# Performance work log

Hardware: AMD Instinct MI355X
Metric: run time of the kernel (lower is better)

## Reference

```python
import jax, jax.numpy as jnp
import numpy as np

N = 100000
E = 1600000
DIN = 128
HID = 128
EPS = 1e-5


def setup_inputs() -> dict:
    key = jax.random.key(0)
    ks = jax.random.split(key, 16)
    s = lambda i, shape, sc=0.05: jax.random.normal(ks[i], shape, dtype=jnp.float32) * sc
    inp = {
        "x": jax.random.normal(ks[0], (N, DIN), dtype=jnp.float32),
        "edge_index": jax.random.randint(ks[1], (2, E), 0, N, dtype=jnp.int64),
        # layer 1
        "W1": s(2, (DIN, HID)), "b1": jnp.zeros((HID,), jnp.float32),
        "g1": jnp.ones((HID,), jnp.float32), "be1": jnp.zeros((HID,), jnp.float32),
        "m1": s(3, (HID,)), "v1": jax.random.uniform(ks[4], (HID,), jnp.float32) + 0.5,
        # layer 2
        "W2": s(5, (HID, HID)), "b2": jnp.zeros((HID,), jnp.float32),
        "g2": jnp.ones((HID,), jnp.float32), "be2": jnp.zeros((HID,), jnp.float32),
        "m2": s(6, (HID,)), "v2": jax.random.uniform(ks[7], (HID,), jnp.float32) + 0.5,
        # classifier
        "Wc1": s(8, (HID, HID // 2)), "bc1": jnp.zeros((HID // 2,), jnp.float32),
        "Wc2": s(9, (HID // 2, 2)), "bc2": jnp.zeros((2,), jnp.float32),
    }
    return inp


def _gnn_layer(x, W, b, src, dst):
    # linear then scatter-mean of source features onto destinations
    h = x @ W + b                                    # [N, HID]
    msg_sum = jax.ops.segment_sum(h[src], dst, num_segments=N)   # [N, HID]
    cnt = jax.ops.segment_sum(jnp.ones((src.shape[0],), h.dtype), dst, num_segments=N)
    return msg_sum / cnt[:, None]                    # self-loops guarantee cnt >= 1


def _bn(x, g, be, m, v):
    return (x - m) * jax.lax.rsqrt(v + EPS) * g + be


def reference(x, edge_index, W1, b1, g1, be1, m1, v1, W2, b2, g2, be2, m2, v2, Wc1, bc1, Wc2, bc2):
    # add self loops (PyG add_self_loops appends [i, i])
    loop = jnp.arange(N, dtype=edge_index.dtype)
    src = jnp.concatenate([edge_index[0], loop])
    dst = jnp.concatenate([edge_index[1], loop])

    h = _gnn_layer(x, W1, b1, src, dst)
    h = jax.nn.relu(_bn(h, g1, be1, m1, v1))
    h = _gnn_layer(h, W2, b2, src, dst)
    h = jax.nn.relu(_bn(h, g2, be2, m2, v2))

    h = jax.nn.relu(h @ Wc1 + bc1)
    return h @ Wc2 + bc2                              # logits [N, 2]
```

## Files before the change

kernel.cpp:

```cpp
#include <hip/hip_runtime.h>
#include <hip/hip_bf16.h>

#define EPS 1e-5f

__global__ __launch_bounds__(256) void k_zero(int* p, int n) {
    int i = blockIdx.x * 256 + threadIdx.x;
    if (i < n) p[i] = 0;
}

__global__ __launch_bounds__(256) void k_histrank(const int* __restrict__ dst,
                                                  int* __restrict__ counts,
                                                  int* __restrict__ rank, int nE) {
    int i = blockIdx.x * 256 + threadIdx.x;
    if (i < nE) rank[i] = atomicAdd(&counts[dst[i]], 1);
}

__global__ __launch_bounds__(256) void k_scan1(const int* __restrict__ counts,
                                               int* __restrict__ bsums, int n) {
    __shared__ int sdata[256];
    int base = blockIdx.x * 2048;
    int t = threadIdx.x;
    int s = 0;
#pragma unroll
    for (int i = 0; i < 8; ++i) {
        int idx = base + t * 8 + i;
        if (idx < n) s += counts[idx];
    }
    sdata[t] = s;
    __syncthreads();
    for (int off = 128; off > 0; off >>= 1) {
        if (t < off) sdata[t] += sdata[t + off];
        __syncthreads();
    }
    if (t == 0) bsums[blockIdx.x] = sdata[0];
}

__global__ __launch_bounds__(64) void k_scan2(int* __restrict__ bsums, int nb) {
    if (threadIdx.x == 0 && blockIdx.x == 0) {
        int acc = 0;
        for (int i = 0; i < nb; ++i) { int v = bsums[i]; bsums[i] = acc; acc += v; }
    }
}

__global__ __launch_bounds__(256) void k_scan3(const int* __restrict__ counts,
                                               const int* __restrict__ bsums,
                                               int* __restrict__ rowstart,
                                               int n, int nE) {
    __shared__ int sth[256];
    int base = blockIdx.x * 2048;
    int t = threadIdx.x;
    int loc[8];
    int s = 0;
#pragma unroll
    for (int i = 0; i < 8; ++i) {
        int idx = base + t * 8 + i;
        loc[i] = s;
        s += (idx < n) ? counts[idx] : 0;
    }
    sth[t] = s;
    __syncthreads();
    for (int off = 1; off < 256; off <<= 1) {
        int tmp = (t >= off) ? sth[t - off] : 0;
        __syncthreads();
        sth[t] += tmp;
        __syncthreads();
    }
    int excl = sth[t] - s + bsums[blockIdx.x];
#pragma unroll
    for (int i = 0; i < 8; ++i) {
        int idx = base + t * 8 + i;
        if (idx < n) rowstart[idx] = excl + loc[i];
    }
    if (blockIdx.x == 0 && t == 0) rowstart[n] = nE;
}

__global__ __launch_bounds__(256) void k_fill3(const int* __restrict__ srci,
                                               const int* __restrict__ dsti,
                                               const int* __restrict__ rank,
                                               const int* __restrict__ rowstart,
                                               int* __restrict__ col, int nE) {
    int e = blockIdx.x * 256 + threadIdx.x;
    if (e < nE) {
        col[rowstart[dsti[e]] + rank[e]] = srci[e];
    }
}

__global__ __launch_bounds__(256) void k_linear(const float* __restrict__ X,
                                                const float* __restrict__ W,
                                                const float* __restrict__ bias,
                                                float* __restrict__ out,
                                                int nRows) {
    __shared__ float xs[64][132];
    int row0 = blockIdx.x * 64;
    int tid = threadIdx.x;
    for (int i = tid; i < 64 * 32; i += 256) {
        int r = i >> 5, c4 = (i & 31) << 2;
        float4 v = make_float4(0.f, 0.f, 0.f, 0.f);
        int row = row0 + r;
        if (row < nRows) v = *(const float4*)(X + (size_t)row * 128 + c4);
        *(float4*)&xs[r][c4] = v;
    }
    __syncthreads();

    int cg = tid & 15, rg = tid >> 4;
    int c0 = cg * 8, r0 = rg * 4;
    float acc[4][8];
    float4 b0 = *(const float4*)(bias + c0);
    float4 b1 = *(const float4*)(bias + c0 + 4);
#pragma unroll
    for (int r = 0; r < 4; ++r) {
        acc[r][0] = b0.x; acc[r][1] = b0.y; acc[r][2] = b0.z; acc[r][3] = b0.w;
        acc[r][4] = b1.x; acc[r][5] = b1.y; acc[r][6] = b1.z; acc[r][7] = b1.w;
    }

    for (int k0 = 0; k0 < 128; k0 += 4) {
        float4 xv[4];
#pragma unroll
        for (int r = 0; r < 4; ++r) xv[r] = *(const float4*)&xs[r0 + r][k0];
#pragma unroll
        for (int kk = 0; kk < 4; ++kk) {
            int k = k0 + kk;
            float4 w0 = *(const float4*)(W + k * 128 + c0);
            float4 w1 = *(const float4*)(W + k * 128 + c0 + 4);
            float wv[8] = {w0.x, w0.y, w0.z, w0.w, w1.x, w1.y, w1.z, w1.w};
#pragma unroll
            for (int r = 0; r < 4; ++r) {
                float xk = (&xv[r].x)[kk];
#pragma unroll
                for (int j = 0; j < 8; ++j) acc[r][j] = fmaf(xk, wv[j], acc[r][j]);
            }
        }
    }

#pragma unroll
    for (int r = 0; r < 4; ++r) {
        int row = row0 + r0 + r;
        if (row >= nRows) continue;
        *(float4*)(out + (size_t)row * 128 + c0) =
            make_float4(acc[r][0], acc[r][1], acc[r][2], acc[r][3]);
        *(float4*)(out + (size_t)row * 128 + c0 + 4) =
            make_float4(acc[r][4], acc[r][5], acc[r][6], acc[r][7]);
    }
}

template <bool FUSE_BN>
__global__ __launch_bounds__(256) void k_gather(const float* __restrict__ src,
                                                const int* __restrict__ rowstart,
                                                const int* __restrict__ col,
                                                const float* __restrict__ g,
                                                const float* __restrict__ be,
                                                const float* __restrict__ m,
                                                const float* __restrict__ v,
                                                float* __restrict__ out, int nRows) {
    int r = blockIdx.x * 4 + (threadIdx.x >> 6);
    if (r >= nRows) return;
    int lane = threadIdx.x & 63;
    int d0 = lane * 2;
    int s = rowstart[r], e = rowstart[r + 1];

    float2 acc = *(const float2*)(src + (size_t)r * 128 + d0);
    int j = s;
    for (; j + 8 <= e; j += 8) {
        int ci[8];
#pragma unroll
        for (int u = 0; u < 8; ++u) ci[u] = col[j + u];
        float2 t[8];
#pragma unroll
        for (int u = 0; u < 8; ++u)
            t[u] = *(const float2*)(src + (size_t)ci[u] * 128 + d0);
#pragma unroll
        for (int u = 0; u < 8; ++u) { acc.x += t[u].x; acc.y += t[u].y; }
    }
    for (; j < e; ++j) {
        int ci = col[j];
        float2 a = *(const float2*)(src + (size_t)ci * 128 + d0);
        acc.x += a.x;
        acc.y += a.y;
    }
    float rc = 1.0f / (float)(e - s + 1);
    float2 o;
    if (FUSE_BN) {
        float2 gv = *(const float2*)(g + d0);
        float2 bev = *(const float2*)(be + d0);
        float2 mv = *(const float2*)(m + d0);
        float2 vv = *(const float2*)(v + d0);
        o.x = fmaxf((acc.x * rc - mv.x) * rsqrtf(vv.x + EPS) * gv.x + bev.x, 0.f);
        o.y = fmaxf((acc.y * rc - mv.y) * rsqrtf(vv.y + EPS) * gv.y + bev.y, 0.f);
    } else {
        o.x = acc.x * rc;
        o.y = acc.y * rc;
    }
    *(float2*)(out + (size_t)r * 128 + d0) = o;
}

__global__ __launch_bounds__(256) void k_final(const float* __restrict__ xin,
                                               const float* __restrict__ Wc1,
                                               const float* __restrict__ bc1,
                                               const float* __restrict__ Wc2,
                                               const float* __restrict__ bc2,
                                               float* __restrict__ out, int nRows) {
    __shared__ float xs[32][132];
    __shared__ float w1s[128][64];
    __shared__ float hs[32][68];
    int row0 = blockIdx.x * 32;
    int tid = threadIdx.x;

    for (int i = tid; i < 2048; i += 256) {
        int kk = i >> 4, c4 = (i & 15) << 2;
        *(float4*)&w1s[kk][c4] = *(const float4*)(Wc1 + kk * 64 + c4);
    }
    for (int i = tid; i < 1024; i += 256) {
        int r = i >> 5, c4 = (i & 31) << 2;
        int row = row0 + r;
        float4 o = make_float4(0.f, 0.f, 0.f, 0.f);
        if (row < nRows) o = *(const float4*)(xin + (size_t)row * 128 + c4);
        *(float4*)&xs[r][c4] = o;
    }
    __syncthreads();

    int cg = tid & 15, rg = tid >> 4;
    int c0 = cg * 4, r0 = rg * 2;
    float acc[2][4];
    float4 bc = *(const float4*)(bc1 + c0);
    acc[0][0] = bc.x; acc[0][1] = bc.y; acc[0][2] = bc.z; acc[0][3] = bc.w;
    acc[1][0] = bc.x; acc[1][1] = bc.y; acc[1][2] = bc.z; acc[1][3] = bc.w;
    for (int k = 0; k < 128; ++k) {
        float4 w4 = *(const float4*)&w1s[k][c0];
        float x0 = xs[r0][k], x1 = xs[r0 + 1][k];
        acc[0][0] = fmaf(x0, w4.x, acc[0][0]);
        acc[0][1] = fmaf(x0, w4.y, acc[0][1]);
        acc[0][2] = fmaf(x0, w4.z, acc[0][2]);
        acc[0][3] = fmaf(x0, w4.w, acc[0][3]);
        acc[1][0] = fmaf(x1, w4.x, acc[1][0]);
        acc[1][1] = fmaf(x1, w4.y, acc[1][1]);
        acc[1][2] = fmaf(x1, w4.z, acc[1][2]);
        acc[1][3] = fmaf(x1, w4.w, acc[1][3]);
    }
    *(float4*)&hs[r0][c0] = make_float4(fmaxf(acc[0][0], 0.f), fmaxf(acc[0][1], 0.f),
                                        fmaxf(acc[0][2], 0.f), fmaxf(acc[0][3], 0.f));
    *(float4*)&hs[r0 + 1][c0] = make_float4(fmaxf(acc[1][0], 0.f), fmaxf(acc[1][1], 0.f),
                                            fmaxf(acc[1][2], 0.f), fmaxf(acc[1][3], 0.f));
    __syncthreads();

    if (tid < 64) {
        int r = tid >> 1, oc = tid & 1;
        float s = bc2[oc];
        for (int c = 0; c < 64; ++c) s = fmaf(hs[r][c], Wc2[c * 2 + oc], s);
        int row = row0 + r;
        if (row < nRows) out[(size_t)row * 2 + oc] = s;
    }
}

extern "C" void kernel_launch(void* const* d_in, const int* in_sizes, int n_in,
                              void* d_out, int out_size, void* d_ws, size_t ws_size,
                              hipStream_t stream) {
    const float* x   = (const float*)d_in[0];
    const int*   ei  = (const int*)d_in[1];
    const float* W1  = (const float*)d_in[2];
    const float* b1  = (const float*)d_in[3];
    const float* g1  = (const float*)d_in[4];
    const float* be1 = (const float*)d_in[5];
    const float* m1  = (const float*)d_in[6];
    const float* v1  = (const float*)d_in[7];
    const float* W2  = (const float*)d_in[8];
    const float* b2  = (const float*)d_in[9];
    const float* g2  = (const float*)d_in[10];
    const float* be2 = (const float*)d_in[11];
    const float* m2  = (const float*)d_in[12];
    const float* v2  = (const float*)d_in[13];
    const float* Wc1 = (const float*)d_in[14];
    const float* bc1 = (const float*)d_in[15];
    const float* Wc2 = (const float*)d_in[16];
    const float* bc2 = (const float*)d_in[17];

    const int N_ = in_sizes[0] / 128;
    const int E_ = in_sizes[1] / 2;
    const int* srci = ei;
    const int* dsti = ei + E_;

    float* A = (float*)d_ws;
    float* B = A + (size_t)N_ * 128;
    int* rank = (int*)B;
    int* counts   = (int*)(B + (size_t)N_ * 128);
    int* rowstart = counts + N_;
    int* bsums    = rowstart + N_ + 1;
    int* col      = bsums + 256;

    const int nb = (N_ + 2047) / 2048;

    k_zero    <<<(N_ + 255) / 256, 256, 0, stream>>>(counts, N_);
    k_histrank<<<(E_ + 255) / 256, 256, 0, stream>>>(dsti, counts, rank, E_);
    k_scan1   <<<nb, 256, 0, stream>>>(counts, bsums, N_);
    k_scan2   <<<1, 64, 0, stream>>>(bsums, nb);
    k_scan3   <<<nb, 256, 0, stream>>>(counts, bsums, rowstart, N_, E_);
    k_fill3   <<<(E_ + 255) / 256, 256, 0, stream>>>(srci, dsti, rank, rowstart,
                                                     col, E_);

    k_linear<<<(N_ + 63) / 64, 256, 0, stream>>>(x, W1, b1, A, N_);
    k_gather<true><<<(N_ + 3) / 4, 256, 0, stream>>>(A, rowstart, col,
                                                     g1, be1, m1, v1, B, N_);

    k_linear<<<(N_ + 63) / 64, 256, 0, stream>>>(B, W2, b2, A, N_);
    k_gather<true><<<(N_ + 3) / 4, 256, 0, stream>>>(A, rowstart, col,
                                                     g2, be2, m2, v2, B, N_);

    k_final<<<(N_ + 31) / 32, 256, 0, stream>>>(B, Wc1, bc1, Wc2, bc2,
                                                (float*)d_out, N_);
}
```

Measured before the change: 630.4 us.

## Fuse gather+BN with next linear layer and with classifier head

Merges each neighbor-gather/batchnorm/relu kernel with the following dense layer (W2 linear, or the two-layer classifier head). Aggregated rows go into shared memory and are multiplied directly, so the intermediate N×128 tensor is no longer written to and re-read from global memory. Weights are now read from global/L1 per k-step instead of being staged in LDS. Also replaces the zeroing kernel with hipMemsetAsync and makes the rank store nontemporal.

```diff
diff --git a/kernel.cpp b/kernel.cpp
--- a/kernel.cpp
+++ b/kernel.cpp
@@ -2,17 +2,15 @@
 #include <hip/hip_bf16.h>
 
 #define EPS 1e-5f
-
-__global__ __launch_bounds__(256) void k_zero(int* p, int n) {
-    int i = blockIdx.x * 256 + threadIdx.x;
-    if (i < n) p[i] = 0;
-}
 
 __global__ __launch_bounds__(256) void k_histrank(const int* __restrict__ dst,
                                                   int* __restrict__ counts,
                                                   int* __restrict__ rank, int nE) {
     int i = blockIdx.x * 256 + threadIdx.x;
-    if (i < nE) rank[i] = atomicAdd(&counts[dst[i]], 1);
+    if (i < nE) {
+        int p = atomicAdd(&counts[dst[i]], 1);
+        __builtin_nontemporal_store(p, &rank[i]);
+    }
 }
 
 __global__ __launch_bounds__(256) void k_scan1(const int* __restrict__ counts,
@@ -143,103 +141,176 @@
     }
 }
 
-template <bool FUSE_BN>
-__global__ __launch_bounds__(256) void k_gather(const float* __restrict__ src,
-                                                const int* __restrict__ rowstart,
-                                                const int* __restrict__ col,
-                                                const float* __restrict__ g,
-                                                const float* __restrict__ be,
-                                                const float* __restrict__ m,
-                                                const float* __restrict__ v,
-                                                float* __restrict__ out, int nRows) {
-    int r = blockIdx.x * 4 + (threadIdx.x >> 6);
-    if (r >= nRows) return;
-    int lane = threadIdx.x & 63;
+__global__ __launch_bounds__(512) void k_glin(const float* __restrict__ src,
+                                              const int* __restrict__ rowstart,
+                                              const int* __restrict__ col,
+                                              const float* __restrict__ g,
+                                              const float* __restrict__ be,
+                                              const float* __restrict__ m,
+                                              const float* __restrict__ v,
+                                              const float* __restrict__ W,
+                                              const float* __restrict__ bias,
+                                              float* __restrict__ out, int nRows) {
+    __shared__ float xs[32][132];
+    int row0 = blockIdx.x * 32;
+    int tid = threadIdx.x;
+    int wid = tid >> 6, lane = tid & 63;
     int d0 = lane * 2;
-    int s = rowstart[r], e = rowstart[r + 1];
-
-    float2 acc = *(const float2*)(src + (size_t)r * 128 + d0);
-    int j = s;
-    for (; j + 8 <= e; j += 8) {
-        int ci[8];
-#pragma unroll
-        for (int u = 0; u < 8; ++u) ci[u] = col[j + u];
-        float2 t[8];
-#pragma unroll
-        for (int u = 0; u < 8; ++u)
-            t[u] = *(const float2*)(src + (size_t)ci[u] * 128 + d0);
-#pragma unroll
-        for (int u = 0; u < 8; ++u) { acc.x += t[u].x; acc.y += t[u].y; }
-    }
-    for (; j < e; ++j) {
-        int ci = col[j];
-        float2 a = *(const float2*)(src + (size_t)ci * 128 + d0);
-        acc.x += a.x;
-        acc.y += a.y;
-    }
-    float rc = 1.0f / (float)(e - s + 1);
-    float2 o;
-    if (FUSE_BN) {
-        float2 gv = *(const float2*)(g + d0);
-        float2 bev = *(const float2*)(be + d0);
-        float2 mv = *(const float2*)(m + d0);
-        float2 vv = *(const float2*)(v + d0);
-        o.x = fmaxf((acc.x * rc - mv.x) * rsqrtf(vv.x + EPS) * gv.x + bev.x, 0.f);
-        o.y = fmaxf((acc.y * rc - mv.y) * rsqrtf(vv.y + EPS) * gv.y + bev.y, 0.f);
-    } else {
-        o.x = acc.x * rc;
-        o.y = acc.y * rc;
-    }
-    *(float2*)(out + (size_t)r * 128 + d0) = o;
-}
-
-__global__ __launch_bounds__(256) void k_final(const float* __restrict__ xin,
+
+    float2 gv  = *(const float2*)(g + d0);
+    float2 bev = *(const float2*)(be + d0);
+    float2 mv  = *(const float2*)(m + d0);
+    float2 vv  = *(const float2*)(v + d0);
+    float sx = rsqrtf(vv.x + EPS) * gv.x;
+    float sy = rsqrtf(vv.y + EPS) * gv.y;
+
+#pragma unroll
+    for (int rr = 0; rr < 4; ++rr) {
+        int lr = wid * 4 + rr;
+        int r = row0 + lr;
+        float2 o = make_float2(0.f, 0.f);
+        if (r < nRows) {
+            int s = rowstart[r], e = rowstart[r + 1];
+            float2 acc = *(const float2*)(src + (size_t)r * 128 + d0);
+            int j = s;
+            for (; j + 8 <= e; j += 8) {
+                int ci[8];
+#pragma unroll
+                for (int u = 0; u < 8; ++u) ci[u] = col[j + u];
+                float2 t[8];
+#pragma unroll
+                for (int u = 0; u < 8; ++u)
+                    t[u] = *(const float2*)(src + (size_t)ci[u] * 128 + d0);
+#pragma unroll
+                for (int u = 0; u < 8; ++u) { acc.x += t[u].x; acc.y += t[u].y; }
+            }
+            for (; j < e; ++j) {
+                int ci = col[j];
+                float2 a = *(const float2*)(src + (size_t)ci * 128 + d0);
+                acc.x += a.x; acc.y += a.y;
+            }
+            float rc = 1.0f / (float)(e - s + 1);
+            o.x = fmaxf((acc.x * rc - mv.x) * sx + bev.x, 0.f);
+            o.y = fmaxf((acc.y * rc - mv.y) * sy + bev.y, 0.f);
+        }
+        *(float2*)&xs[lr][d0] = o;
+    }
+    __syncthreads();
+
+    int cg = tid & 15, rg = tid >> 4;
+    int c0 = cg * 8;
+    float acc[8];
+    float4 b0 = *(const float4*)(bias + c0);
+    float4 b1 = *(const float4*)(bias + c0 + 4);
+    acc[0] = b0.x; acc[1] = b0.y; acc[2] = b0.z; acc[3] = b0.w;
+    acc[4] = b1.x; acc[5] = b1.y; acc[6] = b1.z; acc[7] = b1.w;
+
+    for (int k0 = 0; k0 < 128; k0 += 4) {
+        float4 xv = *(const float4*)&xs[rg][k0];
+#pragma unroll
+        for (int kk = 0; kk < 4; ++kk) {
+            int k = k0 + kk;
+            float4 w0 = *(const float4*)(W + k * 128 + c0);
+            float4 w1 = *(const float4*)(W + k * 128 + c0 + 4);
+            float xk = (&xv.x)[kk];
+            acc[0] = fmaf(xk, w0.x, acc[0]);
+            acc[1] = fmaf(xk, w0.y, acc[1]);
+            acc[2] = fmaf(xk, w0.z, acc[2]);
+            acc[3] = fmaf(xk, w0.w, acc[3]);
+            acc[4] = fmaf(xk, w1.x, acc[4]);
+            acc[5] = fmaf(xk, w1.y, acc[5]);
+            acc[6] = fmaf(xk, w1.z, acc[6]);
+            acc[7] = fmaf(xk, w1.w, acc[7]);
+        }
+    }
+
+    int orow = row0 + rg;
+    if (orow < nRows) {
+        *(float4*)(out + (size_t)orow * 128 + c0) =
+            make_float4(acc[0], acc[1], acc[2], acc[3]);
+        *(float4*)(out + (size_t)orow * 128 + c0 + 4) =
+            make_float4(acc[4], acc[5], acc[6], acc[7]);
+    }
+}
+
+__global__ __launch_bounds__(512) void k_ghead(const float* __restrict__ src,
+                                               const int* __restrict__ rowstart,
+                                               const int* __restrict__ col,
+                                               const float* __restrict__ g,
+                                               const float* __restrict__ be,
+                                               const float* __restrict__ m,
+                                               const float* __restrict__ v,
                                                const float* __restrict__ Wc1,
                                                const float* __restrict__ bc1,
                                                const float* __restrict__ Wc2,
                                                const float* __restrict__ bc2,
                                                float* __restrict__ out, int nRows) {
     __shared__ float xs[32][132];
-    __shared__ float w1s[128][64];
     __shared__ float hs[32][68];
     int row0 = blockIdx.x * 32;
     int tid = threadIdx.x;
-
-    for (int i = tid; i < 2048; i += 256) {
-        int kk = i >> 4, c4 = (i & 15) << 2;
-        *(float4*)&w1s[kk][c4] = *(const float4*)(Wc1 + kk * 64 + c4);
-    }
-    for (int i = tid; i < 1024; i += 256) {
-        int r = i >> 5, c4 = (i & 31) << 2;
-        int row = row0 + r;
-        float4 o = make_float4(0.f, 0.f, 0.f, 0.f);
-        if (row < nRows) o = *(const float4*)(xin + (size_t)row * 128 + c4);
-        *(float4*)&xs[r][c4] = o;
+    int wid = tid >> 6, lane = tid & 63;
+    int d0 = lane * 2;
+
+    float2 gv  = *(const float2*)(g + d0);
+    float2 bev = *(const float2*)(be + d0);
+    float2 mv  = *(const float2*)(m + d0);
+    float2 vv  = *(const float2*)(v + d0);
+    float sx = rsqrtf(vv.x + EPS) * gv.x;
+    float sy = rsqrtf(vv.y + EPS) * gv.y;
+
+#pragma unroll
+    for (int rr = 0; rr < 4; ++rr) {
+        int lr = wid * 4 + rr;
+        int r = row0 + lr;
+        float2 o = make_float2(0.f, 0.f);
+        if (r < nRows) {
+            int s = rowstart[r], e = rowstart[r + 1];
+            float2 acc = *(const float2*)(src + (size_t)r * 128 + d0);
+            int j = s;
+            for (; j + 8 <= e; j += 8) {
+                int ci[8];
+#pragma unroll
+                for (int u = 0; u < 8; ++u) ci[u] = col[j + u];
+                float2 t[8];
+#pragma unroll
+                for (int u = 0; u < 8; ++u)
+                    t[u] = *(const float2*)(src + (size_t)ci[u] * 128 + d0);
+#pragma unroll
+                for (int u = 0; u < 8; ++u) { acc.x += t[u].x; acc.y += t[u].y; }
+            }
+            for (; j < e; ++j) {
+                int ci = col[j];
+                float2 a = *(const float2*)(src + (size_t)ci * 128 + d0);
+                acc.x += a.x; acc.y += a.y;
+            }
+            float rc = 1.0f / (float)(e - s + 1);
+            o.x = fmaxf((acc.x * rc - mv.x) * sx + bev.x, 0.f);
+            o.y = fmaxf((acc.y * rc - mv.y) * sy + bev.y, 0.f);
+        }
+        *(float2*)&xs[lr][d0] = o;
     }
     __syncthreads();
 
     int cg = tid & 15, rg = tid >> 4;
-    int c0 = cg * 4, r0 = rg * 2;
-    float acc[2][4];
+    int c0 = cg * 4;
+    float acc[4];
     float4 bc = *(const float4*)(bc1 + c0);
-    acc[0][0] = bc.x; acc[0][1] = bc.y; acc[0][2] = bc.z; acc[0][3] = bc.w;
-    acc[1][0] = bc.x; acc[1][1] = bc.y; acc[1][2] = bc.z; acc[1][3] = bc.w;
-    for (int k = 0; k < 128; ++k) {
-        float4 w4 = *(const float4*)&w1s[k][c0];
-        float x0 = xs[r0][k], x1 = xs[r0 + 1][k];
-        acc[0][0] = fmaf(x0, w4.x, acc[0][0]);
-        acc[0][1] = fmaf(x0, w4.y, acc[0][1]);
-        acc[0][2] = fmaf(x0, w4.z, acc[0][2]);
-        acc[0][3] = fmaf(x0, w4.w, acc[0][3]);
-        acc[1][0] = fmaf(x1, w4.x, acc[1][0]);
-        acc[1][1] = fmaf(x1, w4.y, acc[1][1]);
-        acc[1][2] = fmaf(x1, w4.z, acc[1][2]);
-        acc[1][3] = fmaf(x1, w4.w, acc[1][3]);
-    }
-    *(float4*)&hs[r0][c0] = make_float4(fmaxf(acc[0][0], 0.f), fmaxf(acc[0][1], 0.f),
-                                        fmaxf(acc[0][2], 0.f), fmaxf(acc[0][3], 0.f));
-    *(float4*)&hs[r0 + 1][c0] = make_float4(fmaxf(acc[1][0], 0.f), fmaxf(acc[1][1], 0.f),
-                                            fmaxf(acc[1][2], 0.f), fmaxf(acc[1][3], 0.f));
+    acc[0] = bc.x; acc[1] = bc.y; acc[2] = bc.z; acc[3] = bc.w;
+    for (int k0 = 0; k0 < 128; k0 += 4) {
+        float4 xv = *(const float4*)&xs[rg][k0];
+#pragma unroll
+        for (int kk = 0; kk < 4; ++kk) {
+            float4 w4 = *(const float4*)(Wc1 + (k0 + kk) * 64 + c0);
+            float xk = (&xv.x)[kk];
+            acc[0] = fmaf(xk, w4.x, acc[0]);
+            acc[1] = fmaf(xk, w4.y, acc[1]);
+            acc[2] = fmaf(xk, w4.z, acc[2]);
+            acc[3] = fmaf(xk, w4.w, acc[3]);
+        }
+    }
+    *(float4*)&hs[rg][c0] = make_float4(fmaxf(acc[0], 0.f), fmaxf(acc[1], 0.f),
+                                        fmaxf(acc[2], 0.f), fmaxf(acc[3], 0.f));
     __syncthreads();
 
     if (tid < 64) {
@@ -288,7 +359,7 @@
 
     const int nb = (N_ + 2047) / 2048;
 
-    k_zero    <<<(N_ + 255) / 256, 256, 0, stream>>>(counts, N_);
+    hipMemsetAsync(counts, 0, (size_t)N_ * sizeof(int), stream);
     k_histrank<<<(E_ + 255) / 256, 256, 0, stream>>>(dsti, counts, rank, E_);
     k_scan1   <<<nb, 256, 0, stream>>>(counts, bsums, N_);
     k_scan2   <<<1, 64, 0, stream>>>(bsums, nb);
@@ -297,13 +368,13 @@
                                                      col, E_);
 
     k_linear<<<(N_ + 63) / 64, 256, 0, stream>>>(x, W1, b1, A, N_);
-    k_gather<true><<<(N_ + 3) / 4, 256, 0, stream>>>(A, rowstart, col,
-                                                     g1, be1, m1, v1, B, N_);
-
-    k_linear<<<(N_ + 63) / 64, 256, 0, stream>>>(B, W2, b2, A, N_);
-    k_gather<true><<<(N_ + 3) / 4, 256, 0, stream>>>(A, rowstart, col,
-                                                     g2, be2, m2, v2, B, N_);
-
-    k_final<<<(N_ + 31) / 32, 256, 0, stream>>>(B, Wc1, bc1, Wc2, bc2,
+
+    k_glin<<<(N_ + 31) / 32, 512, 0, stream>>>(A, rowstart, col,
+                                               g1, be1, m1, v1,
+                                               W2, b2, B, N_);
+
+    k_ghead<<<(N_ + 31) / 32, 512, 0, stream>>>(B, rowstart, col,
+                                                g2, be2, m2, v2,
+                                                Wc1, bc1, Wc2, bc2,
                                                 (float*)d_out, N_);
 }
```

Measured after the change: 816.3 us. 29.5% more time.

## Overlap first-layer linear with CSR histogram and fill kernels via block partitioning

Applied to the files above, without the earlier changes.

The first-layer linear transform is split in half, and each half runs as extra blocks inside the histogram kernel and the CSR fill kernel, so the compute-bound GEMM tiles share the GPU with the atomic- and scatter-bound graph build. The zeroing kernel is replaced with hipMemsetAsync, and rank stores use nontemporal hints. This removes two kernel launches and aims to hide the latency-bound scatter work behind dense compute. The cost is that fused blocks reserve the linear tile's shared memory even for histogram blocks, which may lower occupancy for the atomic phase.

```diff
diff --git a/kernel.cpp b/kernel.cpp
--- a/kernel.cpp
+++ b/kernel.cpp
@@ -3,16 +3,100 @@
 
 #define EPS 1e-5f
 
-__global__ __launch_bounds__(256) void k_zero(int* p, int n) {
-    int i = blockIdx.x * 256 + threadIdx.x;
-    if (i < n) p[i] = 0;
-}
-
-__global__ __launch_bounds__(256) void k_histrank(const int* __restrict__ dst,
+__device__ __forceinline__ void lin_tile(const float* __restrict__ X,
+                                         const float* __restrict__ W,
+                                         const float* __restrict__ bias,
+                                         float* __restrict__ out,
+                                         float (*xs)[132],
+                                         int row0, int rowLim, int tid) {
+    for (int i = tid; i < 64 * 32; i += 256) {
+        int r = i >> 5, c4 = (i & 31) << 2;
+        float4 v = make_float4(0.f, 0.f, 0.f, 0.f);
+        int row = row0 + r;
+        if (row < rowLim) v = *(const float4*)(X + (size_t)row * 128 + c4);
+        *(float4*)&xs[r][c4] = v;
+    }
+    __syncthreads();
+
+    int cg = tid & 15, rg = tid >> 4;
+    int c0 = cg * 8, r0 = rg * 4;
+    float acc[4][8];
+    float4 b0 = *(const float4*)(bias + c0);
+    float4 b1 = *(const float4*)(bias + c0 + 4);
+#pragma unroll
+    for (int r = 0; r < 4; ++r) {
+        acc[r][0] = b0.x; acc[r][1] = b0.y; acc[r][2] = b0.z; acc[r][3] = b0.w;
+        acc[r][4] = b1.x; acc[r][5] = b1.y; acc[r][6] = b1.z; acc[r][7] = b1.w;
+    }
+
+    for (int k0 = 0; k0 < 128; k0 += 4) {
+        float4 xv[4];
+#pragma unroll
+        for (int r = 0; r < 4; ++r) xv[r] = *(const float4*)&xs[r0 + r][k0];
+#pragma unroll
+        for (int kk = 0; kk < 4; ++kk) {
+            int k = k0 + kk;
+            float4 w0 = *(const float4*)(W + k * 128 + c0);
+            float4 w1 = *(const float4*)(W + k * 128 + c0 + 4);
+            float wv[8] = {w0.x, w0.y, w0.z, w0.w, w1.x, w1.y, w1.z, w1.w};
+#pragma unroll
+            for (int r = 0; r < 4; ++r) {
+                float xk = (&xv[r].x)[kk];
+#pragma unroll
+                for (int j = 0; j < 8; ++j) acc[r][j] = fmaf(xk, wv[j], acc[r][j]);
+            }
+        }
+    }
+
+#pragma unroll
+    for (int r = 0; r < 4; ++r) {
+        int row = row0 + r0 + r;
+        if (row >= rowLim) continue;
+        *(float4*)(out + (size_t)row * 128 + c0) =
+            make_float4(acc[r][0], acc[r][1], acc[r][2], acc[r][3]);
+        *(float4*)(out + (size_t)row * 128 + c0 + 4) =
+            make_float4(acc[r][4], acc[r][5], acc[r][6], acc[r][7]);
+    }
+}
+
+__global__ __launch_bounds__(256) void k_hist_lin(const int* __restrict__ dst,
                                                   int* __restrict__ counts,
-                                                  int* __restrict__ rank, int nE) {
-    int i = blockIdx.x * 256 + threadIdx.x;
-    if (i < nE) rank[i] = atomicAdd(&counts[dst[i]], 1);
+                                                  int* __restrict__ rank, int nE, int HB,
+                                                  const float* __restrict__ X,
+                                                  const float* __restrict__ W,
+                                                  const float* __restrict__ bias,
+                                                  float* __restrict__ out, int rowLim1) {
+    __shared__ float xs[64][132];
+    int bid = blockIdx.x;
+    if (bid < HB) {
+        int i = bid * 256 + threadIdx.x;
+        if (i < nE) {
+            int p = atomicAdd(&counts[dst[i]], 1);
+            __builtin_nontemporal_store(p, &rank[i]);
+        }
+    } else {
+        lin_tile(X, W, bias, out, xs, (bid - HB) * 64, rowLim1, threadIdx.x);
+    }
+}
+
+__global__ __launch_bounds__(256) void k_fill_lin(const int* __restrict__ srci,
+                                                  const int* __restrict__ dsti,
+                                                  const int* __restrict__ rank,
+                                                  const int* __restrict__ rowstart,
+                                                  int* __restrict__ col, int nE, int FB,
+                                                  const float* __restrict__ X,
+                                                  const float* __restrict__ W,
+                                                  const float* __restrict__ bias,
+                                                  float* __restrict__ out,
+                                                  int row0_2, int nRows) {
+    __shared__ float xs[64][132];
+    int bid = blockIdx.x;
+    if (bid < FB) {
+        int e = bid * 256 + threadIdx.x;
+        if (e < nE) col[rowstart[dsti[e]] + rank[e]] = srci[e];
+    } else {
+        lin_tile(X, W, bias, out, xs, row0_2 + (bid - FB) * 64, nRows, threadIdx.x);
+    }
 }
 
 __global__ __launch_bounds__(256) void k_scan1(const int* __restrict__ counts,
@@ -74,73 +158,13 @@
     if (blockIdx.x == 0 && t == 0) rowstart[n] = nE;
 }
 
-__global__ __launch_bounds__(256) void k_fill3(const int* __restrict__ srci,
-                                               const int* __restrict__ dsti,
-                                               const int* __restrict__ rank,
-                                               const int* __restrict__ rowstart,
-                                               int* __restrict__ col, int nE) {
-    int e = blockIdx.x * 256 + threadIdx.x;
-    if (e < nE) {
-        col[rowstart[dsti[e]] + rank[e]] = srci[e];
-    }
-}
-
 __global__ __launch_bounds__(256) void k_linear(const float* __restrict__ X,
                                                 const float* __restrict__ W,
                                                 const float* __restrict__ bias,
                                                 float* __restrict__ out,
                                                 int nRows) {
     __shared__ float xs[64][132];
-    int row0 = blockIdx.x * 64;
-    int tid = threadIdx.x;
-    for (int i = tid; i < 64 * 32; i += 256) {
-        int r = i >> 5, c4 = (i & 31) << 2;
-        float4 v = make_float4(0.f, 0.f, 0.f, 0.f);
-        int row = row0 + r;
-        if (row < nRows) v = *(const float4*)(X + (size_t)row * 128 + c4);
-        *(float4*)&xs[r][c4] = v;
-    }
-    __syncthreads();
-
-    int cg = tid & 15, rg = tid >> 4;
-    int c0 = cg * 8, r0 = rg * 4;
-    float acc[4][8];
-    float4 b0 = *(const float4*)(bias + c0);
-    float4 b1 = *(const float4*)(bias + c0 + 4);
-#pragma unroll
-    for (int r = 0; r < 4; ++r) {
-        acc[r][0] = b0.x; acc[r][1] = b0.y; acc[r][2] = b0.z; acc[r][3] = b0.w;
-        acc[r][4] = b1.x; acc[r][5] = b1.y; acc[r][6] = b1.z; acc[r][7] = b1.w;
-    }
-
-    for (int k0 = 0; k0 < 128; k0 += 4) {
-        float4 xv[4];
-#pragma unroll
-        for (int r = 0; r < 4; ++r) xv[r] = *(const float4*)&xs[r0 + r][k0];
-#pragma unroll
-        for (int kk = 0; kk < 4; ++kk) {
-            int k = k0 + kk;
-            float4 w0 = *(const float4*)(W + k * 128 + c0);
-            float4 w1 = *(const float4*)(W + k * 128 + c0 + 4);
-            float wv[8] = {w0.x, w0.y, w0.z, w0.w, w1.x, w1.y, w1.z, w1.w};
-#pragma unroll
-            for (int r = 0; r < 4; ++r) {
-                float xk = (&xv[r].x)[kk];
-#pragma unroll
-                for (int j = 0; j < 8; ++j) acc[r][j] = fmaf(xk, wv[j], acc[r][j]);
-            }
-        }
-    }
-
-#pragma unroll
-    for (int r = 0; r < 4; ++r) {
-        int row = row0 + r0 + r;
-        if (row >= nRows) continue;
-        *(float4*)(out + (size_t)row * 128 + c0) =
-            make_float4(acc[r][0], acc[r][1], acc[r][2], acc[r][3]);
-        *(float4*)(out + (size_t)row * 128 + c0 + 4) =
-            make_float4(acc[r][4], acc[r][5], acc[r][6], acc[r][7]);
-    }
+    lin_tile(X, W, bias, out, xs, blockIdx.x * 64, nRows, threadIdx.x);
 }
 
 template <bool FUSE_BN>
@@ -288,19 +312,28 @@
 
     const int nb = (N_ + 2047) / 2048;
 
-    k_zero    <<<(N_ + 255) / 256, 256, 0, stream>>>(counts, N_);
-    k_histrank<<<(E_ + 255) / 256, 256, 0, stream>>>(dsti, counts, rank, E_);
-    k_scan1   <<<nb, 256, 0, stream>>>(counts, bsums, N_);
-    k_scan2   <<<1, 64, 0, stream>>>(bsums, nb);
-    k_scan3   <<<nb, 256, 0, stream>>>(counts, bsums, rowstart, N_, E_);
-    k_fill3   <<<(E_ + 255) / 256, 256, 0, stream>>>(srci, dsti, rank, rowstart,
-                                                     col, E_);
-
-    k_linear<<<(N_ + 63) / 64, 256, 0, stream>>>(x, W1, b1, A, N_);
+    const int H1  = ((N_ / 2 + 63) / 64) * 64;
+    const int LB1 = H1 / 64;
+    const int LB2 = (N_ - H1 + 63) / 64;
+    const int HB  = (E_ + 255) / 256;
+    const int FB  = HB;
+
+    hipMemsetAsync(counts, 0, (size_t)N_ * sizeof(int), stream);
+
+    k_hist_lin<<<HB + LB1, 256, 0, stream>>>(dsti, counts, rank, E_, HB,
+                                             x, W1, b1, A, H1 < N_ ? H1 : N_);
+    k_scan1<<<nb, 256, 0, stream>>>(counts, bsums, N_);
+    k_scan2<<<1, 64, 0, stream>>>(bsums, nb);
+    k_scan3<<<nb, 256, 0, stream>>>(counts, bsums, rowstart, N_, E_);
+
+    k_fill_lin<<<FB + LB2, 256, 0, stream>>>(srci, dsti, rank, rowstart, col, E_, FB,
+                                             x, W1, b1, A, H1, N_);
+
     k_gather<true><<<(N_ + 3) / 4, 256, 0, stream>>>(A, rowstart, col,
                                                      g1, be1, m1, v1, B, N_);
 
     k_linear<<<(N_ + 63) / 64, 256, 0, stream>>>(B, W2, b2, A, N_);
+
     k_gather<true><<<(N_ + 3) / 4, 256, 0, stream>>>(A, rowstart, col,
                                                      g2, be2, m2, v2, B, N_);
 
```

Result: slower. 655.6 us (+4.0%).
